# Kernel optimization log

Hardware: AMD Instinct MI355X
Metric: run time of the kernel (lower is better)

The kernel has to match this reference:

```python
import jax, jax.numpy as jnp
import numpy as np

VOCAB, CTX, DIMS, HEAD, LAYER = 32000, 1024, 1024, 16, 4
HD = DIMS // HEAD
EPS = 1e-8


def rms_norm(x, w):
    return x * jax.lax.rsqrt(jnp.mean(x * x, axis=-1, keepdims=True) + EPS) * w


def rotary_cos_sin(ctx, inv_freq, bias):
    t = jnp.arange(ctx, dtype=jnp.float32)
    fr = t[:, None] * inv_freq[None, :] + bias[:ctx]  # [S, d/2]
    return jnp.cos(fr), jnp.sin(fr)


def apply_rotary(x, cos, sin):
    # x: [..., S, D]; cos/sin: [S, d2]; rotates first 2*d2 channels (consecutive pairs)
    d2 = cos.shape[-1]
    x1, x2 = x[..., : 2 * d2], x[..., 2 * d2 :]
    a, b = x1[..., 0::2], x1[..., 1::2]
    ra = a * cos - b * sin
    rb = a * sin + b * cos
    x1r = jnp.stack([ra, rb], axis=-1).reshape(x1.shape)
    return jnp.concatenate([x1r, x2], axis=-1)


def attention(x, lna_w, qw, qb, kw, vw, vb, ow, ob, factor, cos, sin):
    B, S, D = x.shape
    h = rms_norm(x, lna_w)
    q = h @ qw.T + qb
    k = h @ kw.T  # k has no bias
    v = h @ vw.T + vb
    split = lambda t: t.reshape(B, S, HEAD, HD).transpose(0, 2, 1, 3)  # [B,H,S,hd]
    q, k, v = split(q), split(k), split(v)
    q = apply_rotary(q, cos, sin)
    k = apply_rotary(k, cos, sin)
    scale = HD ** -0.25
    qk = jnp.einsum('bhqd,bhkd->bhqk', q * scale, k * scale)
    # scaled_mask: 0 above diagonal, 1 elsewhere (multiplicative causal mask, as in source)
    causal = jnp.tril(jnp.ones((S, S), dtype=qk.dtype))
    zero_factor = jnp.clip(jax.nn.softplus(factor), 1e-5, 0.1)
    token_ids = k[..., 0]  # [B,H,S] first key channel
    scaled_zero = jnp.where(token_ids == 0, zero_factor, jnp.ones((), qk.dtype))
    qk = qk * (causal[None, None] * scaled_zero[:, :, None, :])
    w = jax.nn.softmax(qk.astype(jnp.float32), axis=-1)
    out = jnp.einsum('bhqk,bhkd->bhqd', w, v).transpose(0, 2, 1, 3).reshape(B, S, D)
    return out @ ow.T + ob


def reference(x, xa, tok_emb, pos_emb, rot_inv_freq, rot_bias, brot_inv_freq, brot_bias,
              lna_w, q_w, q_b, k_w, v_w, v_b, o_w, o_b, factor, lnc_w,
              mlp_w1, mlp_b1, mlp_w2, mlp_b2, ln_dec_w):
    S = x.shape[1]
    h = tok_emb[x] + pos_emb[:S]  # [B,S,D]; dropout is identity in eval
    cos_d, sin_d = rotary_cos_sin(S, rot_inv_freq, rot_bias)
    h = apply_rotary(h, cos_d, sin_d)
    h = h.astype(xa.dtype)
    cos_b, sin_b = rotary_cos_sin(S, brot_inv_freq, brot_bias)
    for l in range(LAYER):
        r = h
        h = h + attention(h, lna_w[l], q_w[l], q_b[l], k_w[l], v_w[l], v_b[l],
                          o_w[l], o_b[l], factor[l], cos_b, sin_b)
        m = rms_norm(h, lnc_w[l])
        m = jax.nn.relu(m @ mlp_w1[l].T + mlp_b1[l]) @ mlp_w2[l].T + mlp_b2[l]
        h = h + m
        h = h + r  # extra residual from source
    h = rms_norm(h, ln_dec_w)
    logits = h @ tok_emb.T
    return logits


def setup_inputs() -> dict:
    key = jax.random.key(0)
    ks = jax.random.split(key, 16)
    B, S, D, L = 2, CTX, DIMS, LAYER
    tok_emb = 0.02 * jax.random.normal(ks[0], (VOCAB, D), jnp.float32)
    tok_emb = tok_emb.at[0].set(0.0)  # row 0 zeroed as in source
    inp = {
        'x': jax.random.randint(ks[1], (B, S), 0, VOCAB),
        'xa': jax.random.normal(ks[2], (B, S, D), jnp.float32),
        'tok_emb': tok_emb,
        'pos_emb': 0.02 * jax.random.normal(ks[3], (CTX, D), jnp.float32),
        'rot_inv_freq': (1.0 / 10000 ** (jnp.arange(0, D, 2, dtype=jnp.float32) / D)),
        'rot_bias': jnp.zeros((CTX, D // 2), jnp.float32),
        'brot_inv_freq': (1.0 / 10000 ** (jnp.arange(0, HD, 2, dtype=jnp.float32) / HD)),
        'brot_bias': jnp.zeros((CTX, HD // 2), jnp.float32),
        'lna_w': jnp.ones((L, D), jnp.float32),
        'q_w': 0.02 * jax.random.normal(ks[4], (L, D, D), jnp.float32),
        'q_b': jnp.zeros((L, D), jnp.float32),
        'k_w': 0.02 * jax.random.normal(ks[5], (L, D, D), jnp.float32),
        'v_w': 0.02 * jax.random.normal(ks[6], (L, D, D), jnp.float32),
        'v_b': jnp.zeros((L, D), jnp.float32),
        'o_w': 0.02 * jax.random.normal(ks[7], (L, D, D), jnp.float32),
        'o_b': jnp.zeros((L, D), jnp.float32),
        'factor': 0.001 * jnp.ones((L,), jnp.float32),
        'lnc_w': jnp.ones((L, D), jnp.float32),
        'mlp_w1': 0.02 * jax.random.normal(ks[8], (L, 4 * D, D), jnp.float32),
        'mlp_b1': jnp.zeros((L, 4 * D), jnp.float32),
        'mlp_w2': 0.02 * jax.random.normal(ks[9], (L, D, 4 * D), jnp.float32),
        'mlp_b2': jnp.zeros((L, D), jnp.float32),
        'ln_dec_w': jnp.ones((D,), jnp.float32),
    }
    return inp
```

## Files before the change

### kernel.cpp

```cpp
#include <hip/hip_runtime.h>
#include <hip/hip_bf16.h>

#define DD 1024
#define HEADS 16
#define HDIM 64
#define NLAYER 4
#define FFDIM 4096
#define NVOCAB 32000
#define SEQ 1024

typedef __bf16 bf16_t;
typedef __bf16 bf16x8 __attribute__((ext_vector_type(8)));
typedef __bf16 bf16x4 __attribute__((ext_vector_type(4)));
typedef float f32x4 __attribute__((ext_vector_type(4)));

#define MFMA16(a, b, c) __builtin_amdgcn_mfma_f32_16x16x32_bf16((a), (b), (c), 0, 0, 0)

#define GLD16(gp, lp) \
    __builtin_amdgcn_global_load_lds( \
        (const __attribute__((address_space(1))) void*)(gp), \
        (__attribute__((address_space(3))) void*)(lp), 16, 0, 0)

#define BAR() do { __builtin_amdgcn_sched_barrier(0); \
                   __builtin_amdgcn_s_barrier(); \
                   __builtin_amdgcn_sched_barrier(0); } while (0)
#define WAITVM(n) asm volatile("s_waitcnt vmcnt(" #n ")" ::: "memory")

static __device__ __forceinline__ bf16x8 pack8(float4 u, float4 v) {
    bf16x8 r;
    r[0] = (bf16_t)u.x; r[1] = (bf16_t)u.y; r[2] = (bf16_t)u.z; r[3] = (bf16_t)u.w;
    r[4] = (bf16_t)v.x; r[5] = (bf16_t)v.y; r[6] = (bf16_t)v.z; r[7] = (bf16_t)v.w;
    return r;
}

struct CvtBatch {
    const float* src[7];
    bf16_t*      dst[7];
    int          blk0[7];
    int          nseg;
};

__global__ __launch_bounds__(256) void cvt_batch(CvtBatch cb) {
    const int b = blockIdx.x;
    int s = 0;
    #pragma unroll
    for (int t = 1; t < 7; ++t)
        if (t < cb.nseg && b >= cb.blk0[t]) s = t;
    const long i = ((long)(b - cb.blk0[s]) * 256 + threadIdx.x) * 16;
    float4 a0 = *(const float4*)(cb.src[s] + i);
    float4 a1 = *(const float4*)(cb.src[s] + i + 4);
    float4 a2 = *(const float4*)(cb.src[s] + i + 8);
    float4 a3 = *(const float4*)(cb.src[s] + i + 12);
    *(bf16x8*)(cb.dst[s] + i)     = pack8(a0, a1);
    *(bf16x8*)(cb.dst[s] + i + 8) = pack8(a2, a3);
}

__global__ __launch_bounds__(256) void ropetab_kernel(
    const float* __restrict__ inv_freq, const float* __restrict__ rbias,
    float* __restrict__ ctab, float* __restrict__ stab)
{
    int idx = blockIdx.x * 256 + threadIdx.x;
    int s = idx >> 5, i = idx & 31;
    float fr = (float)s * inv_freq[i] + rbias[idx];
    ctab[idx] = cosf(fr);
    stab[idx] = sinf(fr);
}

__global__ __launch_bounds__(512) void embed_rope_kernel(
    const int* __restrict__ x, const float* __restrict__ tok_emb,
    const float* __restrict__ pos_emb, const float* __restrict__ inv_freq,
    const float* __restrict__ rbias, float* __restrict__ h, int S)
{
    const int row = blockIdx.x;
    const int s = row % S;
    const int i = threadIdx.x;
    const int tok = x[row];
    const float* e = tok_emb + (size_t)tok * DD;
    const float* p = pos_emb + (size_t)s * DD;
    float a = e[2*i]   + p[2*i];
    float b = e[2*i+1] + p[2*i+1];
    float fr = (float)s * inv_freq[i] + rbias[(size_t)s * (DD/2) + i];
    float c = cosf(fr), sn = sinf(fr);
    h[(size_t)row*DD + 2*i]   = a*c - b*sn;
    h[(size_t)row*DD + 2*i+1] = a*sn + b*c;
}

__global__ __launch_bounds__(256) void rmsnorm_kernel(
    const float* __restrict__ x, const float* __restrict__ w,
    bf16_t* __restrict__ y)
{
    const int row = blockIdx.x;
    const float* xr = x + (size_t)row * DD;
    float ss = 0.f;
    for (int j = threadIdx.x; j < DD; j += 256) { float v = xr[j]; ss += v*v; }
    for (int off = 32; off > 0; off >>= 1) ss += __shfl_down(ss, off, 64);
    __shared__ float r[4];
    if ((threadIdx.x & 63) == 0) r[threadIdx.x >> 6] = ss;
    __syncthreads();
    float tot = r[0] + r[1] + r[2] + r[3];
    float sc = rsqrtf(tot * (1.0f/(float)DD) + 1e-8f);
    for (int j = threadIdx.x; j < DD; j += 256)
        y[(size_t)row*DD + j] = (bf16_t)(xr[j] * sc * w[j]);
}

__global__ __launch_bounds__(256) void gemm_bf_s(
    const bf16_t* __restrict__ A, const bf16_t* __restrict__ W,
    const float* __restrict__ bias, const float* __restrict__ add1,
    const float* __restrict__ add2, float* __restrict__ C,
    bf16_t* __restrict__ Cb,
    int M, int N, int K, int relu, int mode)
{
    __shared__ __align__(16) bf16_t As[64*64];
    __shared__ __align__(16) bf16_t Bs[128*64];
    const int tid = threadIdx.x;
    const int m0 = blockIdx.y * 64, n0 = blockIdx.x * 128;
    const int l = tid & 63, w = tid >> 6;
    const int wr = (w >> 1) * 32, wc = (w & 1) * 64;
    const int lr = l & 15, lk = (l >> 4) * 8;
    const int swz = (lr & 7) << 3;

    const int srow = l >> 3;
    const int scolS = 8 * ((l & 7) ^ (l >> 3));
    const bf16_t* Ag = A + (size_t)(m0 + w*16 + srow) * K + scolS;
    const bf16_t* Wg = W + (size_t)(n0 + w*32 + srow) * K + scolS;

    f32x4 z4 = {0.f, 0.f, 0.f, 0.f};
    f32x4 acc[2][4];
    #pragma unroll
    for (int i = 0; i < 2; ++i)
        #pragma unroll
        for (int j = 0; j < 4; ++j) acc[i][j] = z4;

    #pragma unroll
    for (int it = 0; it < 2; ++it)
        GLD16(Ag + (size_t)(it*8)*K, As + (w*2 + it)*512);
    #pragma unroll
    for (int it = 0; it < 4; ++it)
        GLD16(Wg + (size_t)(it*8)*K, Bs + (w*4 + it)*512);

    for (int k0 = 0; k0 < K; k0 += 64) {
        __syncthreads();
        bf16x8 afr[4], bfr[8];
        #pragma unroll
        for (int kk = 0; kk < 2; ++kk) {
            #pragma unroll
            for (int i = 0; i < 2; ++i)
                afr[kk*2+i] = *(const bf16x8*)&As[(wr + i*16 + lr)*64 + ((kk*32 + lk) ^ swz)];
            #pragma unroll
            for (int j = 0; j < 4; ++j)
                bfr[kk*4+j] = *(const bf16x8*)&Bs[(wc + j*16 + lr)*64 + ((kk*32 + lk) ^ swz)];
        }
        __syncthreads();
        if (k0 + 64 < K) {
            #pragma unroll
            for (int it = 0; it < 2; ++it)
                GLD16(Ag + (size_t)(it*8)*K + k0 + 64, As + (w*2 + it)*512);
            #pragma unroll
            for (int it = 0; it < 4; ++it)
                GLD16(Wg + (size_t)(it*8)*K + k0 + 64, Bs + (w*4 + it)*512);
        }
        #pragma unroll
        for (int kk = 0; kk < 2; ++kk)
            #pragma unroll
            for (int i = 0; i < 2; ++i)
                #pragma unroll
                for (int j = 0; j < 4; ++j)
                    acc[i][j] = MFMA16(afr[kk*2+i], bfr[kk*4+j], acc[i][j]);
    }

    #pragma unroll
    for (int i = 0; i < 2; ++i) {
        #pragma unroll
        for (int j = 0; j < 4; ++j) {
            const int col  = n0 + wc + j*16 + lr;
            const int row0 = m0 + wr + i*16 + (l >> 4)*4;
            const float bv = bias ? bias[col] : 0.f;
            #pragma unroll
            for (int r2 = 0; r2 < 4; ++r2) {
                const int row = row0 + r2;
                float val = acc[i][j][r2] + bv;
                if (add1) val += add1[(size_t)row*N + col];
                if (add2) val += add2[(size_t)row*N + col];
                if (relu) val = fmaxf(val, 0.f);
                if (mode == 0) C[(size_t)row*N + col] = val;
                else           Cb[(size_t)row*N + col] = (bf16_t)val;
            }
        }
    }
}

__global__ __launch_bounds__(256) void gemm_bf_s64(
    const bf16_t* __restrict__ A, const bf16_t* __restrict__ W,
    const float* __restrict__ bias, const float* __restrict__ add1,
    const float* __restrict__ add2, float* __restrict__ C,
    int M, int N, int K)
{
    __shared__ __align__(16) bf16_t As[2][64*64];
    __shared__ __align__(16) bf16_t Bs[2][64*64];
    const int tid = threadIdx.x;
    const int nbx = gridDim.x, nby = gridDim.y;
    const int nwg = nbx * nby;
    const int lin = blockIdx.y * nbx + blockIdx.x;
    const int wg  = (lin & 7) * (nwg >> 3) + (lin >> 3);
    const int m0 = (wg % nby) * 64, n0 = (wg / nby) * 64;
    const int l = tid & 63, w = tid >> 6;
    const int wr = (w >> 1) * 32, wc = (w & 1) * 32;
    const int lr = l & 15, lk = (l >> 4) * 8;
    const int swz = (lr & 7) << 3;

    const int srow = l >> 3;
    const int scolS = 8 * ((l & 7) ^ (l >> 3));
    const bf16_t* Ag = A + (size_t)(m0 + w*16 + srow) * K + scolS;
    const bf16_t* Wg = W + (size_t)(n0 + w*16 + srow) * K + scolS;

    f32x4 z4 = {0.f, 0.f, 0.f, 0.f};
    f32x4 acc[2][2];
    #pragma unroll
    for (int i = 0; i < 2; ++i)
        #pragma unroll
        for (int j = 0; j < 2; ++j) acc[i][j] = z4;

    auto STAGE2 = [&](int k0) {
        #pragma unroll
        for (int hh = 0; hh < 2; ++hh)
            #pragma unroll
            for (int it = 0; it < 2; ++it) {
                GLD16(Ag + (size_t)(it*8)*K + k0 + hh*64, &As[hh][(w*2 + it)*512]);
                GLD16(Wg + (size_t)(it*8)*K + k0 + hh*64, &Bs[hh][(w*2 + it)*512]);
            }
    };

    STAGE2(0);
    for (int k0 = 0; k0 < K; k0 += 128) {
        __syncthreads();
        bf16x8 afr[2][4], bfr[2][4];
        #pragma unroll
        for (int hh = 0; hh < 2; ++hh)
            #pragma unroll
            for (int kk = 0; kk < 2; ++kk)
                #pragma unroll
                for (int i = 0; i < 2; ++i) {
                    afr[hh][kk*2+i] = *(const bf16x8*)&As[hh][(wr + i*16 + lr)*64 + ((kk*32 + lk) ^ swz)];
                    bfr[hh][kk*2+i] = *(const bf16x8*)&Bs[hh][(wc + i*16 + lr)*64 + ((kk*32 + lk) ^ swz)];
                }
        __syncthreads();
        if (k0 + 128 < K) STAGE2(k0 + 128);
        #pragma unroll
        for (int hh = 0; hh < 2; ++hh)
            #pragma unroll
            for (int kk = 0; kk < 2; ++kk)
                #pragma unroll
                for (int i = 0; i < 2; ++i)
                    #pragma unroll
                    for (int j = 0; j < 2; ++j)
                        acc[i][j] = MFMA16(afr[hh][kk*2+i], bfr[hh][kk*2+j], acc[i][j]);
    }

    #pragma unroll
    for (int i = 0; i < 2; ++i) {
        #pragma unroll
        for (int j = 0; j < 2; ++j) {
            const int col  = n0 + wc + j*16 + lr;
            const int row0 = m0 + wr + i*16 + (l >> 4)*4;
            const float bv = bias ? bias[col] : 0.f;
            #pragma unroll
            for (int r2 = 0; r2 < 4; ++r2) {
                const int row = row0 + r2;
                float val = acc[i][j][r2] + bv;
                if (add1) val += add1[(size_t)row*N + col];
                if (add2) val += add2[(size_t)row*N + col];
                C[(size_t)row*N + col] = val;
            }
        }
    }
}

__global__ __launch_bounds__(512, 2) void gemm256_bf(
    const bf16_t* __restrict__ A, const bf16_t* __restrict__ W,
    float* __restrict__ C, int M, int N)
{
    extern __shared__ __align__(16) char dynsm[];
    bf16_t* TILE = (bf16_t*)dynsm;
    const int tid = threadIdx.x;
    const int nbx = gridDim.x, nby = gridDim.y;
    const int nwg = nbx * nby;
    const int lin = blockIdx.y * nbx + blockIdx.x;
    const int wg  = (lin & 7) * (nwg >> 3) + (lin >> 3);
    const int n0 = (wg / nby) * 256, m0 = (wg % nby) * 256;

    const int l = tid & 63, w = tid >> 6;
    const int wm = w >> 2, wn = w & 3;
    const int lr = l & 15, lg = l >> 4;
    const int swzr = ((l >> 1) & 7) << 3;
    const int srow = tid >> 3;
    const int scolE = ((tid & 7) * 8) ^ (((tid >> 4) & 7) << 3);

    const bf16_t* Ap = A + (size_t)m0 * 1024;
    const bf16_t* Wp = W + (size_t)n0 * 1024;

    auto STG = [&](int buf, int isB, int half, int k0) {
        const bf16_t* G = isB ? Wp : Ap;
        bf16_t* L = TILE + (buf*2 + isB)*16384 + half*8192 + w*512;
        const int rbase = half*128 + srow;
        GLD16(G + (size_t)rbase*1024 + k0 + scolE,          L);
        GLD16(G + (size_t)(rbase + 64)*1024 + k0 + scolE,   L + 4096);
    };
    auto RD_A = [&](int buf, int fi, int kk) -> bf16x8 {
        const int row = wm*128 + fi*16 + lr;
        return *(const bf16x8*)&TILE[(buf*2)*16384 + row*64 + ((kk*32 + lg*8) ^ swzr)];
    };
    auto RD_B = [&](int buf, int fj, int kk) -> bf16x8 {
        const int row = wn*64 + fj*16 + lr;
        return *(const bf16x8*)&TILE[(buf*2 + 1)*16384 + row*64 + ((kk*32 + lg*8) ^ swzr)];
    };

    f32x4 z4 = {0.f, 0.f, 0.f, 0.f};
    f32x4 acc[8][4];
    #pragma unroll
    for (int i = 0; i < 8; ++i)
        #pragma unroll
        for (int j = 0; j < 4; ++j) acc[i][j] = z4;
    bf16x8 bfr[4][2];

#define DO_PHASE(BUF, P, STAGE_STMT, TAIL_STMT) do {                          \
    bf16x8 a0_0 = RD_A(BUF, 2*(P), 0),   a0_1 = RD_A(BUF, 2*(P), 1);          \
    bf16x8 a1_0 = RD_A(BUF, 2*(P)+1, 0), a1_1 = RD_A(BUF, 2*(P)+1, 1);        \
    if ((P) == 0) {                                                           \
        _Pragma("unroll")                                                     \
        for (int fj = 0; fj < 4; ++fj) {                                      \
            bfr[fj][0] = RD_B(BUF, fj, 0);                                    \
            bfr[fj][1] = RD_B(BUF, fj, 1);                                    \
        }                                                                     \
    }                                                                         \
    STAGE_STMT;                                                               \
    BAR();                                                                    \
    __builtin_amdgcn_s_setprio(1);                                            \
    _Pragma("unroll")                                                         \
    for (int fj = 0; fj < 4; ++fj) {                                          \
        acc[2*(P)][fj]   = MFMA16(a0_0, bfr[fj][0], acc[2*(P)][fj]);          \
        acc[2*(P)][fj]   = MFMA16(a0_1, bfr[fj][1], acc[2*(P)][fj]);          \
        acc[2*(P)+1][fj] = MFMA16(a1_0, bfr[fj][0], acc[2*(P)+1][fj]);        \
        acc[2*(P)+1][fj] = MFMA16(a1_1, bfr[fj][1], acc[2*(P)+1][fj]);        \
    }                                                                         \
    __builtin_amdgcn_s_setprio(0);                                            \
    TAIL_STMT;                                                                \
    BAR();                                                                    \
} while (0)

    STG(0, 0, 0, 0);  STG(0, 0, 1, 0);
    STG(0, 1, 0, 0);  STG(0, 1, 1, 0);
    STG(1, 1, 0, 64); STG(1, 1, 1, 64);
    WAITVM(4);
    BAR();

    #pragma unroll 1
    for (int itr = 0; itr < 8; ++itr) {
        const int k_o  = (2*itr + 1) * 64;
        const int k_e2 = (2*itr + 2) * 64;
        const int k_o2 = (2*itr + 3) * 64;
        const bool more = (itr < 7);
        DO_PHASE(0, 0, STG(1, 0, 0, k_o), ;);
        DO_PHASE(0, 1, STG(1, 0, 1, k_o), ;);
        DO_PHASE(0, 2, if (more) STG(0, 1, 0, k_e2), ;);
        DO_PHASE(0, 3, if (more) STG(0, 1, 1, k_e2),
                 if (more) { WAITVM(4); } else { WAITVM(0); });
        DO_PHASE(1, 0, if (more) STG(0, 0, 0, k_e2), ;);
        DO_PHASE(1, 1, if (more) STG(0, 0, 1, k_e2), ;);
        DO_PHASE(1, 2, if (more) STG(1, 1, 0, k_o2), ;);
        DO_PHASE(1, 3, if (more) STG(1, 1, 1, k_o2),
                 if (more) { WAITVM(4); });
    }
#undef DO_PHASE

    #pragma unroll
    for (int i = 0; i < 8; ++i) {
        #pragma unroll
        for (int j = 0; j < 4; ++j) {
            const int col  = n0 + wn*64 + j*16 + lr;
            const int row0 = m0 + wm*128 + i*16 + lg*4;
            #pragma unroll
            for (int r2 = 0; r2 < 4; ++r2)
                C[(size_t)(row0 + r2)*N + col] = acc[i][j][r2];
        }
    }
}

__global__ __launch_bounds__(256) void gemm_bfw32(
    const bf16_t* __restrict__ A, const float* __restrict__ W,
    float* __restrict__ C, int M, int N, int K)
{
    __shared__ __align__(16) bf16_t As[128*64];
    __shared__ __align__(16) bf16_t Bs[128*64];
    const int tid = threadIdx.x;
    const int m0 = blockIdx.y * 128, n0 = blockIdx.x * 128;
    const int l = tid & 63, w = tid >> 6;
    const int wr = (w >> 1) * 64, wc = (w & 1) * 64;
    const int lr = l & 15, lk = (l >> 4) * 8;
    const int srow = l >> 3, scol = (l & 7) * 8;
    const bf16_t* Ag = A + (size_t)(m0 + w*32 + srow) * K + scol;
    const int r = tid >> 1, half = (tid & 1) * 32;
    const float* Wp = W + (size_t)(n0 + r) * K + half;

    f32x4 z4 = {0.f, 0.f, 0.f, 0.f};
    f32x4 acc[4][4];
    #pragma unroll
    for (int i = 0; i < 4; ++i)
        #pragma unroll
        for (int j = 0; j < 4; ++j) acc[i][j] = z4;

    for (int k0 = 0; k0 < K; k0 += 64) {
        float4 wv[8];
        #pragma unroll
        for (int j = 0; j < 8; ++j) wv[j] = *(const float4*)(Wp + k0 + 4*j);
        __syncthreads();
        #pragma unroll
        for (int it = 0; it < 4; ++it)
            GLD16(Ag + (size_t)(it*8)*K + k0, As + (w*4 + it)*512);
        #pragma unroll
        for (int j = 0; j < 4; ++j)
            *(bf16x8*)&Bs[r*64 + half + 8*j] = pack8(wv[2*j], wv[2*j+1]);
        __syncthreads();
        #pragma unroll
        for (int kk = 0; kk < 2; ++kk) {
            bf16x8 afr[4], bfr[4];
            #pragma unroll
            for (int i = 0; i < 4; ++i)
                afr[i] = *(const bf16x8*)&As[(wr + i*16 + lr)*64 + kk*32 + lk];
            #pragma unroll
            for (int j = 0; j < 4; ++j)
                bfr[j] = *(const bf16x8*)&Bs[(wc + j*16 + lr)*64 + kk*32 + lk];
            #pragma unroll
            for (int i = 0; i < 4; ++i)
                #pragma unroll
                for (int j = 0; j < 4; ++j)
                    acc[i][j] = MFMA16(afr[i], bfr[j], acc[i][j]);
        }
    }
    #pragma unroll
    for (int i = 0; i < 4; ++i)
        #pragma unroll
        for (int j = 0; j < 4; ++j) {
            const int col  = n0 + wc + j*16 + lr;
            const int row0 = m0 + wr + i*16 + (l >> 4)*4;
            #pragma unroll
            for (int r2 = 0; r2 < 4; ++r2)
                C[(size_t)(row0 + r2)*N + col] = acc[i][j][r2];
        }
}

__global__ __launch_bounds__(256) void qkv_gemm(
    const bf16_t* __restrict__ A, const bf16_t* __restrict__ Wq,
    const bf16_t* __restrict__ Wk, const bf16_t* __restrict__ Wv,
    const float* __restrict__ qb, const float* __restrict__ vbias,
    const float* __restrict__ ctab, const float* __restrict__ stab,
    const float* __restrict__ fptr,
    bf16_t* __restrict__ qbf, bf16_t* __restrict__ kbf,
    bf16_t* __restrict__ vt, int S)
{
    __shared__ __align__(16) bf16_t smem[2][12288];
    const int tid = threadIdx.x;
    const int seg = blockIdx.x >> 3;
    const int n0  = (blockIdx.x & 7) * 128;
    const int m0  = blockIdx.y * 64;
    const bf16_t* W = (seg == 0) ? Wq : (seg == 1) ? Wk : Wv;
    const int K = DD;
    const int l = tid & 63, w = tid >> 6;
    const int wr = (w >> 1) * 32, wc = (w & 1) * 64;
    const int lr = l & 15, lk = (l >> 4) * 8;
    const int g4 = l >> 4;
    const int swz = (lr & 7) << 3;

    const int srow = l >> 3;
    const int scolS = 8 * ((l & 7) ^ (l >> 3));
    const bf16_t* Ag = A + (size_t)(m0 + w*16 + srow) * K + scolS;
    const bf16_t* Wg = W + (size_t)(n0 + w*32 + srow) * K + scolS;

    f32x4 z4 = {0.f, 0.f, 0.f, 0.f};
    f32x4 acc[2][4];
    #pragma unroll
    for (int i = 0; i < 2; ++i)
        #pragma unroll
        for (int j = 0; j < 4; ++j) acc[i][j] = z4;

    auto STAGE2 = [&](int k0) {
        #pragma unroll
        for (int hh = 0; hh < 2; ++hh) {
            #pragma unroll
            for (int it = 0; it < 2; ++it)
                GLD16(Ag + (size_t)(it*8)*K + k0 + hh*64, &smem[hh][(w*2 + it)*512]);
            #pragma unroll
            for (int it = 0; it < 4; ++it)
                GLD16(Wg + (size_t)(it*8)*K + k0 + hh*64, &smem[hh][4096 + (w*4 + it)*512]);
        }
    };

    STAGE2(0);
    for (int k0 = 0; k0 < K; k0 += 128) {
        __syncthreads();
        bf16x8 afr[2][4], bfr[2][8];
        #pragma unroll
        for (int hh = 0; hh < 2; ++hh)
            #pragma unroll
            for (int kk = 0; kk < 2; ++kk) {
                #pragma unroll
                for (int i = 0; i < 2; ++i)
                    afr[hh][kk*2+i] = *(const bf16x8*)&smem[hh][(wr + i*16 + lr)*64 + ((kk*32 + lk) ^ swz)];
                #pragma unroll
                for (int j = 0; j < 4; ++j)
                    bfr[hh][kk*4+j] = *(const bf16x8*)&smem[hh][4096 + (wc + j*16 + lr)*64 + ((kk*32 + lk) ^ swz)];
            }
        __syncthreads();
        if (k0 + 128 < K) STAGE2(k0 + 128);
        #pragma unroll
        for (int hh = 0; hh < 2; ++hh)
            #pragma unroll
            for (int kk = 0; kk < 2; ++kk)
                #pragma unroll
                for (int i = 0; i < 2; ++i)
                    #pragma unroll
                    for (int j = 0; j < 4; ++j)
                        acc[i][j] = MFMA16(afr[hh][kk*2+i], bfr[hh][kk*4+j], acc[i][j]);
    }

    float zf = 0.f;
    if (seg == 1) {
        float f = fptr[0];
        float sp = (f > 20.f) ? f : log1pf(expf(f));
        zf = fminf(fmaxf(sp, 1e-5f), 0.1f);
    }
    bf16_t* tr = &smem[0][0];

    #pragma unroll
    for (int i = 0; i < 2; ++i) {
        float ov[4][4];
        #pragma unroll
        for (int j = 0; j < 4; ++j) {
            const int col = n0 + wc + j*16 + lr;
            const float bv = (seg == 0) ? qb[col] : (seg == 2) ? vbias[col] : 0.f;
            const int d  = col & 63;
            const int pi = d >> 1;
            #pragma unroll
            for (int r2 = 0; r2 < 4; ++r2) {
                const int row = m0 + wr + i*16 + g4*4 + r2;
                const int s  = row & (SEQ - 1);
                float val = acc[i][j][r2] + bv;
                if (seg < 2) {
                    float partner = __shfl_xor(val, 1, 64);
                    float c  = ctab[s*32 + pi];
                    float sn = stab[s*32 + pi];
                    val = ((d & 1) == 0) ? (val*c - partner*sn)
                                         : (partner*sn + val*c);
                }
                ov[j][r2] = val;
            }
        }
        if (seg == 1) {
            #pragma unroll
            for (int r2 = 0; r2 < 4; ++r2) {
                float z0 = __shfl(ov[0][r2], (l & 48), 64);
                float zr = (z0 == 0.0f) ? zf : 1.0f;
                #pragma unroll
                for (int j = 0; j < 4; ++j) ov[j][r2] *= zr;
            }
        }
        #pragma unroll
        for (int j = 0; j < 4; ++j) {
            const int col = n0 + wc + j*16 + lr;
            #pragma unroll
            for (int r2 = 0; r2 < 4; ++r2) {
                const int row = m0 + wr + i*16 + g4*4 + r2;
                if (seg == 0)      qbf[(size_t)row*DD + col] = (bf16_t)ov[j][r2];
                else if (seg == 1) kbf[(size_t)row*DD + col] = (bf16_t)ov[j][r2];
                else tr[(col - n0)*66 + (row - m0)] = (bf16_t)ov[j][r2];
            }
        }
    }

    if (seg == 2) {
        __syncthreads();
        const int bb2 = m0 >> 10, s0 = m0 & (SEQ - 1);
        const int d2 = tid >> 1, sh = (tid & 1) * 32;
        const int hh2 = (n0 >> 6) + (d2 >> 6);
        const int dd2 = d2 & 63;
        bf16_t* dst = vt + ((size_t)(bb2*HEADS + hh2)*HDIM + dd2)*S + s0 + sh;
        const bf16_t* srcp = tr + d2*66 + sh;
        #pragma unroll
        for (int k2 = 0; k2 < 4; ++k2)
            *(bf16x8*)(dst + k2*8) = *(const bf16x8*)(srcp + k2*8);
    }
}

__global__ __launch_bounds__(256) void attn_fused(
    const bf16_t* __restrict__ qbf, const bf16_t* __restrict__ kbf,
    const bf16_t* __restrict__ Vt, bf16_t* __restrict__ O, int S)
{
    __shared__ __align__(16) bf16_t Ks[2][128*64];
    __shared__ __align__(16) bf16_t Vs[2][64*128];
    __shared__ __align__(16) bf16_t Ps[64*128];

    const int tid = threadIdx.x;
    const int qt = (gridDim.x - 1) - blockIdx.x;
    const int q0 = qt * 64;
    const int bh = blockIdx.y, b = bh >> 4, hh = bh & 15;
    const int l = tid & 63, w = tid >> 6;
    const int lr = l & 15, g = l >> 4;
    const int lk = g * 8;
    const int swz = (lr & 7) << 3;
    const int ktm = q0 >> 7;
    const int cnt = S - 128*(ktm + 1);
    const int myq = q0 + w*16 + lr;
    const int qloc = w*16 + lr;

    bf16x8 qfr[2];
    {
        const bf16_t* qp = qbf + (size_t)(b*S + myq)*DD + hh*HDIM;
        qfr[0] = *(const bf16x8*)(qp + lk);
        qfr[1] = *(const bf16x8*)(qp + 32 + lk);
    }

    float m_run = (cnt > 0) ? 0.f : -3.0e38f;
    float psum = 0.f;
    f32x4 z4 = {0.f, 0.f, 0.f, 0.f};
    f32x4 acc[4];
    #pragma unroll
    for (int j = 0; j < 4; ++j) acc[j] = z4;

    const int sr = l >> 3;
    const int scK = 8 * ((l & 7) ^ (l >> 3));
    const int scV0 = (lr * 8) ^ ((4*0 + g) << 3);
    const int scV1 = (lr * 8) ^ ((4*1 + g) << 3);

    auto STAGEKV = [&](int buf, int kt) {
        const bf16_t* Kg = kbf + (size_t)(b*S + kt*128)*DD + hh*HDIM;
        #pragma unroll
        for (int it = 0; it < 4; ++it) {
            const int krow = (w*4 + it)*8 + sr;
            GLD16(Kg + (size_t)krow*DD + scK, &Ks[buf][(w*4 + it)*512]);
        }
        const bf16_t* Vg = Vt + ((size_t)bh*HDIM)*S + kt*128;
        #pragma unroll
        for (int it = 0; it < 4; ++it) {
            const int drow = (w*4 + it)*4 + g;
            GLD16(Vg + (size_t)drow*S + ((it & 1) ? scV1 : scV0),
                  &Vs[buf][(w*4 + it)*512]);
        }
    };

    for (int kt0 = 0; kt0 <= ktm; kt0 += 2) {
        __syncthreads();
        STAGEKV(0, kt0);
        if (kt0 + 1 <= ktm) STAGEKV(1, kt0 + 1);
        __syncthreads();

        #pragma unroll
        for (int half = 0; half < 2; ++half) {
            const int kt = kt0 + half;
            if (kt > ktm) continue;

            float sv[8][4];
            float mtile = -3.0e38f;
            #pragma unroll
            for (int f = 0; f < 8; ++f) {
                bf16x8 ka0 = *(const bf16x8*)&Ks[half][(f*16 + lr)*64 + (lk ^ swz)];
                bf16x8 ka1 = *(const bf16x8*)&Ks[half][(f*16 + lr)*64 + ((32 + lk) ^ swz)];
                f32x4 t = z4;
                t = MFMA16(ka0, qfr[0], t);
                t = MFMA16(ka1, qfr[1], t);
                #pragma unroll
                for (int r = 0; r < 4; ++r) {
                    const int key = kt*128 + f*16 + g*4 + r;
                    float v = t[r] * 0.125f;
                    v = (key <= myq) ? v : 0.f;
                    sv[f][r] = v;
                    mtile = fmaxf(mtile, v);
                }
            }
            mtile = fmaxf(mtile, __shfl_xor(mtile, 16, 64));
            mtile = fmaxf(mtile, __shfl_xor(mtile, 32, 64));
            const float m_new = fmaxf(m_run, mtile);
            const float fac = expf(m_run - m_new);
            m_run = m_new;

            float ps_t = 0.f;
            #pragma unroll
            for (int f = 0; f < 8; ++f) {
                bf16x4 pk;
                #pragma unroll
                for (int r = 0; r < 4; ++r) {
                    float p = expf(sv[f][r] - m_new);
                    ps_t += p;
                    pk[r] = (bf16_t)p;
                }
                const int byteoff = (qloc*256 + f*32 + g*8) ^ ((lr & 7) << 4);
                *(bf16x4*)((char*)Ps + byteoff) = pk;
            }
            ps_t += __shfl_xor(ps_t, 16, 64);
            ps_t += __shfl_xor(ps_t, 32, 64);
            psum = psum * fac + ps_t;

            #pragma unroll
            for (int r = 0; r < 4; ++r) {
                const float fr_ = __shfl(fac, g*4 + r, 64);
                #pragma unroll
                for (int j = 0; j < 4; ++j) acc[j][r] *= fr_;
            }

            #pragma unroll
            for (int kk = 0; kk < 4; ++kk) {
                const int rboff = (qloc*256 + kk*64 + g*16) ^ ((lr & 7) << 4);
                bf16x8 pa = *(const bf16x8*)((char*)Ps + rboff);
                #pragma unroll
                for (int j = 0; j < 4; ++j) {
                    bf16x8 vb = *(const bf16x8*)&Vs[half][(j*16 + lr)*128 + ((kk*32 + lk) ^ swz)];
                    acc[j] = MFMA16(pa, vb, acc[j]);
                }
            }
        }
    }

    float vtail = 0.f;
    if (cnt > 0) {
        psum += (float)cnt * expf(-m_run);
        const bf16_t* vp = Vt + ((size_t)bh*HDIM + l)*S + 128*(ktm + 1);
        for (int k = 0; k < cnt; k += 8) {
            bf16x8 v = *(const bf16x8*)(vp + k);
            #pragma unroll
            for (int e = 0; e < 8; ++e) vtail += (float)v[e];
        }
    }

    #pragma unroll
    for (int r = 0; r < 4; ++r) {
        const float m_r  = __shfl(m_run, g*4 + r, 64);
        const float ps_r = __shfl(psum,  g*4 + r, 64);
        const float inv = 1.0f / ps_r;
        const float tailf = (cnt > 0) ? expf(-m_r) : 0.f;
        const int qrow = q0 + w*16 + g*4 + r;
        const size_t rowbase = (size_t)(b*S + qrow)*DD + hh*HDIM;
        #pragma unroll
        for (int j = 0; j < 4; ++j) {
            const float vt_j = __shfl(vtail, j*16 + lr, 64);
            float val = acc[j][r];
            if (cnt > 0) val += tailf * vt_j;
            O[rowbase + j*16 + lr] = (bf16_t)(val * inv);
        }
    }
}

extern "C" void kernel_launch(void* const* d_in, const int* in_sizes, int n_in,
                              void* d_out, int out_size, void* d_ws, size_t ws_size,
                              hipStream_t stream)
{
    const int S = SEQ;
    const int B = in_sizes[0] / S;
    const int M = B * S;
    const int BH = B * HEADS;

    const int*   x       = (const int*)  d_in[0];
    const float* tok_emb = (const float*)d_in[2];
    const float* pos_emb = (const float*)d_in[3];
    const float* rif     = (const float*)d_in[4];
    const float* rbias   = (const float*)d_in[5];
    const float* brif    = (const float*)d_in[6];
    const float* bbias   = (const float*)d_in[7];
    const float* lna     = (const float*)d_in[8];
    const float* qw      = (const float*)d_in[9];
    const float* qb      = (const float*)d_in[10];
    const float* kw      = (const float*)d_in[11];
    const float* vw      = (const float*)d_in[12];
    const float* vbias   = (const float*)d_in[13];
    const float* ow      = (const float*)d_in[14];
    const float* ob      = (const float*)d_in[15];
    const float* factor  = (const float*)d_in[16];
    const float* lnc     = (const float*)d_in[17];
    const float* w1      = (const float*)d_in[18];
    const float* b1      = (const float*)d_in[19];
    const float* w2      = (const float*)d_in[20];
    const float* b2      = (const float*)d_in[21];
    const float* lnd     = (const float*)d_in[22];

    char* ob_ = (char*)d_out;
    const size_t MiB = 1024*1024;
    float*  h      = (float*)(ob_ + 0*MiB);
    float*  h2     = (float*)(ob_ + 8*MiB);
    bf16_t* qbf    = (bf16_t*)(ob_ + 16*MiB);
    bf16_t* kbf    = (bf16_t*)(ob_ + 20*MiB);
    bf16_t* vt     = (bf16_t*)(ob_ + 24*MiB);
    bf16_t* attno  = (bf16_t*)(ob_ + 28*MiB);
    bf16_t* m1     = (bf16_t*)(ob_ + 32*MiB);
    float*  ctab   = (float*)(ob_ + 50*MiB);
    float*  stab   = (float*)(ob_ + 51*MiB);
    bf16_t* qw_bf  = (bf16_t*)(ob_ + 64*MiB);
    bf16_t* kw_bf  = (bf16_t*)(ob_ + 72*MiB);
    bf16_t* vw_bf  = (bf16_t*)(ob_ + 80*MiB);
    bf16_t* ow_bf  = (bf16_t*)(ob_ + 88*MiB);
    bf16_t* w1_bf  = (bf16_t*)(ob_ + 96*MiB);
    bf16_t* w2_bf  = (bf16_t*)(ob_ + 128*MiB);

    bf16_t* hn      = (bf16_t*)d_ws;
    bf16_t* temb_bf = (bf16_t*)((char*)d_ws + 4*MiB);
    const bool big_ws = ws_size >= (size_t)(70*MiB);

    {
        CvtBatch cb;
        const float* srcs[7] = {qw, kw, vw, ow, w1, w2, tok_emb};
        bf16_t*      dsts[7] = {qw_bf, kw_bf, vw_bf, ow_bf, w1_bf, w2_bf, temb_bf};
        const long   ns[7]   = {(long)NLAYER*DD*DD, (long)NLAYER*DD*DD,
                                (long)NLAYER*DD*DD, (long)NLAYER*DD*DD,
                                (long)NLAYER*FFDIM*DD, (long)NLAYER*FFDIM*DD,
                                (long)NVOCAB*DD};
        int nseg = big_ws ? 7 : 6;
        int acc = 0;
        for (int s = 0; s < 7; ++s) {
            cb.src[s] = srcs[s]; cb.dst[s] = dsts[s];
            cb.blk0[s] = acc;
            if (s < nseg) acc += (int)(ns[s] / 4096);
        }
        cb.nseg = nseg;
        cvt_batch<<<acc, 256, 0, stream>>>(cb);
    }
    ropetab_kernel<<<(S*32)/256, 256, 0, stream>>>(brif, bbias, ctab, stab);

    dim3 gMLP1(FFDIM/128, M/64);
    dim3 gS64(DD/64,    M/64);
    dim3 gV256(NVOCAB/256, M/256);
    dim3 gVfb(NVOCAB/128, M/128);
    dim3 gQKV(3*8, M/64);
    dim3 gATT(S/64, BH);

    embed_rope_kernel<<<M, 512, 0, stream>>>(x, tok_emb, pos_emb, rif, rbias, h, S);

    for (int l = 0; l < NLAYER; ++l) {
        const size_t wo = (size_t)l * DD * DD;
        const size_t fo = (size_t)l * FFDIM * DD;
        rmsnorm_kernel<<<M, 256, 0, stream>>>(h, lna + l*DD, hn);
        qkv_gemm<<<gQKV, 256, 0, stream>>>(hn, qw_bf + wo, kw_bf + wo, vw_bf + wo,
                                           qb + l*DD, vbias + l*DD, ctab, stab,
                                           factor + l, qbf, kbf, vt, S);
        attn_fused<<<gATT, 256, 0, stream>>>(qbf, kbf, vt, attno, S);
        gemm_bf_s64<<<gS64, 256, 0, stream>>>(attno, ow_bf + wo, ob + l*DD, h, nullptr,
                                              h2, M, DD, DD);
        rmsnorm_kernel<<<M, 256, 0, stream>>>(h2, lnc + l*DD, hn);
        gemm_bf_s<<<gMLP1, 256, 0, stream>>>(hn, w1_bf + fo, b1 + l*FFDIM, nullptr,
                                             nullptr, nullptr, m1, M, FFDIM, DD, 1, 1);
        gemm_bf_s64<<<gS64, 256, 0, stream>>>(m1, w2_bf + fo, b2 + l*DD, h2, h,
                                              h, M, DD, FFDIM);
    }

    rmsnorm_kernel<<<M, 256, 0, stream>>>(h, lnd, hn);
    if (big_ws) {
        hipFuncSetAttribute((const void*)gemm256_bf,
                            hipFuncAttributeMaxDynamicSharedMemorySize, 131072);
        gemm256_bf<<<gV256, 512, 131072, stream>>>(hn, temb_bf, (float*)d_out,
                                                   M, NVOCAB);
    } else {
        gemm_bfw32<<<gVfb, 256, 0, stream>>>(hn, tok_emb, (float*)d_out, M, NVOCAB, DD);
    }
}
```

Before: 895.3 us.

## Store residual stream activations in bf16 instead of fp32

The residual hidden state buffers h and h2 become bf16 instead of fp32. The embedding, rmsnorm and out-proj/MLP2 epilogues now read and write bf16, and rmsnorm uses vectorized 4-element loads. Unused add operands are also dropped from gemm_bf_s. This halves residual memory traffic but adds rounding to the residual at every layer, which risks accuracy drift.

```diff
diff --git a/kernel.cpp b/kernel.cpp
--- a/kernel.cpp
+++ b/kernel.cpp
@@ -12,6 +12,7 @@
 typedef __bf16 bf16_t;
 typedef __bf16 bf16x8 __attribute__((ext_vector_type(8)));
 typedef __bf16 bf16x4 __attribute__((ext_vector_type(4)));
+typedef __bf16 bf16x2 __attribute__((ext_vector_type(2)));
 typedef float f32x4 __attribute__((ext_vector_type(4)));
 
 #define MFMA16(a, b, c) __builtin_amdgcn_mfma_f32_16x16x32_bf16((a), (b), (c), 0, 0, 0)
@@ -69,7 +70,7 @@
 __global__ __launch_bounds__(512) void embed_rope_kernel(
     const int* __restrict__ x, const float* __restrict__ tok_emb,
     const float* __restrict__ pos_emb, const float* __restrict__ inv_freq,
-    const float* __restrict__ rbias, float* __restrict__ h, int S)
+    const float* __restrict__ rbias, bf16_t* __restrict__ h, int S)
 {
     const int row = blockIdx.x;
     const int s = row % S;
@@ -81,32 +82,38 @@
     float b = e[2*i+1] + p[2*i+1];
     float fr = (float)s * inv_freq[i] + rbias[(size_t)s * (DD/2) + i];
     float c = cosf(fr), sn = sinf(fr);
-    h[(size_t)row*DD + 2*i]   = a*c - b*sn;
-    h[(size_t)row*DD + 2*i+1] = a*sn + b*c;
+    bf16x2 o;
+    o[0] = (bf16_t)(a*c - b*sn);
+    o[1] = (bf16_t)(a*sn + b*c);
+    *(bf16x2*)(h + (size_t)row*DD + 2*i) = o;
 }
 
 __global__ __launch_bounds__(256) void rmsnorm_kernel(
-    const float* __restrict__ x, const float* __restrict__ w,
+    const bf16_t* __restrict__ x, const float* __restrict__ w,
     bf16_t* __restrict__ y)
 {
     const int row = blockIdx.x;
-    const float* xr = x + (size_t)row * DD;
-    float ss = 0.f;
-    for (int j = threadIdx.x; j < DD; j += 256) { float v = xr[j]; ss += v*v; }
+    const int j0 = threadIdx.x * 4;
+    bf16x4 xv = *(const bf16x4*)(x + (size_t)row*DD + j0);
+    float v0 = (float)xv[0], v1 = (float)xv[1], v2 = (float)xv[2], v3 = (float)xv[3];
+    float ss = v0*v0 + v1*v1 + v2*v2 + v3*v3;
     for (int off = 32; off > 0; off >>= 1) ss += __shfl_down(ss, off, 64);
     __shared__ float r[4];
     if ((threadIdx.x & 63) == 0) r[threadIdx.x >> 6] = ss;
     __syncthreads();
     float tot = r[0] + r[1] + r[2] + r[3];
     float sc = rsqrtf(tot * (1.0f/(float)DD) + 1e-8f);
-    for (int j = threadIdx.x; j < DD; j += 256)
-        y[(size_t)row*DD + j] = (bf16_t)(xr[j] * sc * w[j]);
+    bf16x4 o;
+    o[0] = (bf16_t)(v0 * sc * w[j0 + 0]);
+    o[1] = (bf16_t)(v1 * sc * w[j0 + 1]);
+    o[2] = (bf16_t)(v2 * sc * w[j0 + 2]);
+    o[3] = (bf16_t)(v3 * sc * w[j0 + 3]);
+    *(bf16x4*)(y + (size_t)row*DD + j0) = o;
 }
 
 __global__ __launch_bounds__(256) void gemm_bf_s(
     const bf16_t* __restrict__ A, const bf16_t* __restrict__ W,
-    const float* __restrict__ bias, const float* __restrict__ add1,
-    const float* __restrict__ add2, float* __restrict__ C,
+    const float* __restrict__ bias, float* __restrict__ C,
     bf16_t* __restrict__ Cb,
     int M, int N, int K, int relu, int mode)
 {
@@ -179,8 +186,6 @@
             for (int r2 = 0; r2 < 4; ++r2) {
                 const int row = row0 + r2;
                 float val = acc[i][j][r2] + bv;
-                if (add1) val += add1[(size_t)row*N + col];
-                if (add2) val += add2[(size_t)row*N + col];
                 if (relu) val = fmaxf(val, 0.f);
                 if (mode == 0) C[(size_t)row*N + col] = val;
                 else           Cb[(size_t)row*N + col] = (bf16_t)val;
@@ -191,8 +196,8 @@
 
 __global__ __launch_bounds__(256) void gemm_bf_s64(
     const bf16_t* __restrict__ A, const bf16_t* __restrict__ W,
-    const float* __restrict__ bias, const float* __restrict__ add1,
-    const float* __restrict__ add2, float* __restrict__ C,
+    const float* __restrict__ bias, const bf16_t* __restrict__ add1,
+    const bf16_t* __restrict__ add2, bf16_t* __restrict__ C,
     int M, int N, int K)
 {
     __shared__ __align__(16) bf16_t As[2][64*64];
@@ -267,9 +272,9 @@
             for (int r2 = 0; r2 < 4; ++r2) {
                 const int row = row0 + r2;
                 float val = acc[i][j][r2] + bv;
-                if (add1) val += add1[(size_t)row*N + col];
-                if (add2) val += add2[(size_t)row*N + col];
-                C[(size_t)row*N + col] = val;
+                if (add1) val += (float)add1[(size_t)row*N + col];
+                if (add2) val += (float)add2[(size_t)row*N + col];
+                C[(size_t)row*N + col] = (bf16_t)val;
             }
         }
     }
@@ -781,8 +786,8 @@
 
     char* ob_ = (char*)d_out;
     const size_t MiB = 1024*1024;
-    float*  h      = (float*)(ob_ + 0*MiB);
-    float*  h2     = (float*)(ob_ + 8*MiB);
+    bf16_t* h      = (bf16_t*)(ob_ + 0*MiB);
+    bf16_t* h2     = (bf16_t*)(ob_ + 8*MiB);
     bf16_t* qbf    = (bf16_t*)(ob_ + 16*MiB);
     bf16_t* kbf    = (bf16_t*)(ob_ + 20*MiB);
     bf16_t* vt     = (bf16_t*)(ob_ + 24*MiB);
@@ -841,8 +846,8 @@
         gemm_bf_s64<<<gS64, 256, 0, stream>>>(attno, ow_bf + wo, ob + l*DD, h, nullptr,
                                               h2, M, DD, DD);
         rmsnorm_kernel<<<M, 256, 0, stream>>>(h2, lnc + l*DD, hn);
-        gemm_bf_s<<<gMLP1, 256, 0, stream>>>(hn, w1_bf + fo, b1 + l*FFDIM, nullptr,
-                                             nullptr, nullptr, m1, M, FFDIM, DD, 1, 1);
+        gemm_bf_s<<<gMLP1, 256, 0, stream>>>(hn, w1_bf + fo, b1 + l*FFDIM,
+                                             nullptr, m1, M, FFDIM, DD, 1, 1);
         gemm_bf_s64<<<gS64, 256, 0, stream>>>(m1, w2_bf + fo, b2 + l*DD, h2, h,
                                               h, M, DD, FFDIM);
     }
```

Measured after the change: 868.6 us. -3.0%, faster.
